# Kernel optimization log

Hardware: AMD Instinct MI355X
Metric: run time of the kernel (lower is better)

Reference implementation:

```python
import jax, jax.numpy as jnp
import numpy as np

N = 8192  # input_size
DT = 1.0
TAU1, TAU2, TAU3 = 20.0, 50.0, 100.0


def _corr(a, b):
    # Pearson correlation of two equal-length vectors (torch.corrcoef[0,1]), NaN -> 0
    ac = a - jnp.mean(a)
    bc = b - jnp.mean(b)
    c = jnp.sum(ac * bc) / jnp.sqrt(jnp.sum(ac * ac) * jnp.sum(bc * bc))
    return jnp.where(jnp.isnan(c), jnp.zeros_like(c), c)


def setup_inputs() -> dict:
    key = jax.random.key(0)
    ks = jax.random.split(key, 8)
    return {
        'sensory_motor_input': jax.random.normal(ks[0], (N,), jnp.float32),
        'layer1_state': jax.random.normal(ks[1], (N,), jnp.float32),
        'layer2_state': jax.random.normal(ks[2], (N // 2,), jnp.float32),
        'layer3_state': jax.random.normal(ks[3], (N // 4,), jnp.float32),
        'w12': jax.random.normal(ks[4], (N // 2, N), jnp.float32) * 0.1,
        'w23': jax.random.normal(ks[5], (N // 4, N // 2), jnp.float32) * 0.1,
        'w32': jax.random.normal(ks[6], (N // 2, N // 4), jnp.float32) * 0.1,
        'w21': jax.random.normal(ks[7], (N, N // 2), jnp.float32) * 0.1,
        'correlation_strength': jnp.zeros((), jnp.float32),
        'neural_coherence': jnp.zeros((), jnp.float32),
    }


def reference(sensory_motor_input, layer1_state, layer2_state, layer3_state,
              w12, w23, w32, w21, correlation_strength, neural_coherence):
    # Layer 1: direct sensorimotor, exponential decay toward tanh target
    l1_target = jnp.tanh(sensory_motor_input)
    d1 = 1.0 - DT / TAU1
    l1 = d1 * layer1_state + (1.0 - d1) * l1_target

    # Layer 2: bottom-up + 0.3 * top-down feedback
    l2_in = w12 @ l1 + 0.3 * (w32 @ layer3_state)
    d2 = 1.0 - DT / TAU2
    l2 = d2 * layer2_state + (1.0 - d2) * jnp.tanh(l2_in)

    # Layer 3: meta feedback
    d3 = 1.0 - DT / TAU3
    l3 = d3 * layer3_state + (1.0 - d3) * jnp.tanh(w23 @ l2)

    # Cross-layer correlations (truncate the larger vector)
    c12 = _corr(l1[: l2.shape[0]], l2)
    c23 = _corr(l2[: l3.shape[0]], l3)
    corr_new = 0.9 * correlation_strength + 0.1 * (c12 + c23) / 2.0

    total_activity = jnp.sum(jnp.abs(l1)) + jnp.sum(jnp.abs(l2)) + jnp.sum(jnp.abs(l3))
    activity_variance = jnp.var(jnp.concatenate([l1, l2, l3]), ddof=1)  # torch.var unbiased
    coherence = total_activity / (activity_variance + 1e-6)
    coh_new = 0.9 * neural_coherence + 0.1 * jnp.clip(coherence, 0.0, 10.0)

    hier_activity = total_activity / (N + N // 2 + N // 4)
    return (l1, l2, l3, corr_new, coh_new, hier_activity)
```

## Files before the change

### kernel.cpp

```cpp
#include <hip/hip_runtime.h>
#include <math.h>

#define N1 8192
#define N2 4096
#define N3 2048

typedef float f4 __attribute__((ext_vector_type(4)));

__global__ __launch_bounds__(256) void k_pre(const float* __restrict__ smi,
                                             const float* __restrict__ l1s,
                                             float* __restrict__ l1,
                                             const float* __restrict__ w32,
                                             const float* __restrict__ l3s,
                                             float* __restrict__ t2) {
    const int b = blockIdx.x;
    const int t = threadIdx.x;
    if (b < 32) {
        const int i = b * 256 + t;
        l1[i] = 0.95f * l1s[i] + 0.05f * tanhf(smi[i]);
        return;
    }
    __shared__ float ws[4][4];
    const int r0 = (b - 32) * 4;
    const f4* __restrict__ w0 = reinterpret_cast<const f4*>(w32) + (size_t)r0 * (N3 / 4);
    const f4* __restrict__ w1 = w0 + (N3 / 4);
    const f4* __restrict__ w2 = w1 + (N3 / 4);
    const f4* __restrict__ w3 = w2 + (N3 / 4);
    const f4* __restrict__ x = reinterpret_cast<const f4*>(l3s);

    float a0 = 0.f, a1 = 0.f, a2 = 0.f, a3 = 0.f;
#pragma unroll
    for (int k = 0; k < (N3 / 4) / 256; ++k) {
        const int i = t + k * 256;
        f4 xv = x[i];
        f4 u0 = __builtin_nontemporal_load(&w0[i]);
        f4 u1 = __builtin_nontemporal_load(&w1[i]);
        f4 u2 = __builtin_nontemporal_load(&w2[i]);
        f4 u3 = __builtin_nontemporal_load(&w3[i]);
        a0 = fmaf(u0.x, xv.x, fmaf(u0.y, xv.y, fmaf(u0.z, xv.z, fmaf(u0.w, xv.w, a0))));
        a1 = fmaf(u1.x, xv.x, fmaf(u1.y, xv.y, fmaf(u1.z, xv.z, fmaf(u1.w, xv.w, a1))));
        a2 = fmaf(u2.x, xv.x, fmaf(u2.y, xv.y, fmaf(u2.z, xv.z, fmaf(u2.w, xv.w, a2))));
        a3 = fmaf(u3.x, xv.x, fmaf(u3.y, xv.y, fmaf(u3.z, xv.z, fmaf(u3.w, xv.w, a3))));
    }
#pragma unroll
    for (int off = 32; off; off >>= 1) {
        a0 += __shfl_down(a0, off, 64);
        a1 += __shfl_down(a1, off, 64);
        a2 += __shfl_down(a2, off, 64);
        a3 += __shfl_down(a3, off, 64);
    }
    if ((t & 63) == 0) {
        const int w = t >> 6;
        ws[w][0] = a0; ws[w][1] = a1; ws[w][2] = a2; ws[w][3] = a3;
    }
    __syncthreads();
    if (t < 4) {
        t2[r0 + t] = ws[0][t] + ws[1][t] + ws[2][t] + ws[3][t];
    }
}

__global__ __launch_bounds__(256) void k_l2(const float* __restrict__ w12,
                                            const float* __restrict__ l1,
                                            const float* __restrict__ t2,
                                            const float* __restrict__ l2s,
                                            float* __restrict__ l2) {
    __shared__ float ws[4][4];
    const int r0 = blockIdx.x * 4;
    const int t = threadIdx.x;
    const f4* __restrict__ w0 = reinterpret_cast<const f4*>(w12) + (size_t)r0 * (N1 / 4);
    const f4* __restrict__ w1 = w0 + (N1 / 4);
    const f4* __restrict__ w2 = w1 + (N1 / 4);
    const f4* __restrict__ w3 = w2 + (N1 / 4);
    const f4* __restrict__ x = reinterpret_cast<const f4*>(l1);

    float a0 = 0.f, a1 = 0.f, a2 = 0.f, a3 = 0.f;
#pragma unroll
    for (int k = 0; k < (N1 / 4) / 256; ++k) {
        const int i = t + k * 256;
        f4 xv = x[i];
        f4 u0 = __builtin_nontemporal_load(&w0[i]);
        f4 u1 = __builtin_nontemporal_load(&w1[i]);
        f4 u2 = __builtin_nontemporal_load(&w2[i]);
        f4 u3 = __builtin_nontemporal_load(&w3[i]);
        a0 = fmaf(u0.x, xv.x, fmaf(u0.y, xv.y, fmaf(u0.z, xv.z, fmaf(u0.w, xv.w, a0))));
        a1 = fmaf(u1.x, xv.x, fmaf(u1.y, xv.y, fmaf(u1.z, xv.z, fmaf(u1.w, xv.w, a1))));
        a2 = fmaf(u2.x, xv.x, fmaf(u2.y, xv.y, fmaf(u2.z, xv.z, fmaf(u2.w, xv.w, a2))));
        a3 = fmaf(u3.x, xv.x, fmaf(u3.y, xv.y, fmaf(u3.z, xv.z, fmaf(u3.w, xv.w, a3))));
    }
#pragma unroll
    for (int off = 32; off; off >>= 1) {
        a0 += __shfl_down(a0, off, 64);
        a1 += __shfl_down(a1, off, 64);
        a2 += __shfl_down(a2, off, 64);
        a3 += __shfl_down(a3, off, 64);
    }
    if ((t & 63) == 0) {
        const int w = t >> 6;
        ws[w][0] = a0; ws[w][1] = a1; ws[w][2] = a2; ws[w][3] = a3;
    }
    __syncthreads();
    if (t < 4) {
        const int r = r0 + t;
        float tot = ws[0][t] + ws[1][t] + ws[2][t] + ws[3][t] + 0.3f * t2[r];
        l2[r] = 0.98f * l2s[r] + 0.02f * tanhf(tot);
    }
}

__global__ __launch_bounds__(256) void k_l3(const float* __restrict__ w23,
                                            const float* __restrict__ l2,
                                            const float* __restrict__ l3s,
                                            float* __restrict__ l3) {
    __shared__ float ws[4][4];
    const int r0 = blockIdx.x * 4;
    const int t = threadIdx.x;
    const f4* __restrict__ w0 = reinterpret_cast<const f4*>(w23) + (size_t)r0 * (N2 / 4);
    const f4* __restrict__ w1 = w0 + (N2 / 4);
    const f4* __restrict__ w2 = w1 + (N2 / 4);
    const f4* __restrict__ w3 = w2 + (N2 / 4);
    const f4* __restrict__ x = reinterpret_cast<const f4*>(l2);

    float a0 = 0.f, a1 = 0.f, a2 = 0.f, a3 = 0.f;
#pragma unroll
    for (int k = 0; k < (N2 / 4) / 256; ++k) {
        const int i = t + k * 256;
        f4 xv = x[i];
        f4 u0 = __builtin_nontemporal_load(&w0[i]);
        f4 u1 = __builtin_nontemporal_load(&w1[i]);
        f4 u2 = __builtin_nontemporal_load(&w2[i]);
        f4 u3 = __builtin_nontemporal_load(&w3[i]);
        a0 = fmaf(u0.x, xv.x, fmaf(u0.y, xv.y, fmaf(u0.z, xv.z, fmaf(u0.w, xv.w, a0))));
        a1 = fmaf(u1.x, xv.x, fmaf(u1.y, xv.y, fmaf(u1.z, xv.z, fmaf(u1.w, xv.w, a1))));
        a2 = fmaf(u2.x, xv.x, fmaf(u2.y, xv.y, fmaf(u2.z, xv.z, fmaf(u2.w, xv.w, a2))));
        a3 = fmaf(u3.x, xv.x, fmaf(u3.y, xv.y, fmaf(u3.z, xv.z, fmaf(u3.w, xv.w, a3))));
    }
#pragma unroll
    for (int off = 32; off; off >>= 1) {
        a0 += __shfl_down(a0, off, 64);
        a1 += __shfl_down(a1, off, 64);
        a2 += __shfl_down(a2, off, 64);
        a3 += __shfl_down(a3, off, 64);
    }
    if ((t & 63) == 0) {
        const int w = t >> 6;
        ws[w][0] = a0; ws[w][1] = a1; ws[w][2] = a2; ws[w][3] = a3;
    }
    __syncthreads();
    if (t < 4) {
        const int r = r0 + t;
        float tot = ws[0][t] + ws[1][t] + ws[2][t] + ws[3][t];
        l3[r] = 0.99f * l3s[r] + 0.01f * tanhf(tot);
    }
}

__global__ __launch_bounds__(1024) void k_fin(const float* __restrict__ out,
                                              const float* __restrict__ corr_in,
                                              const float* __restrict__ coh_in,
                                              float* __restrict__ scal) {
    __shared__ double sred[16][13];
    __shared__ double fin[13];
    const int t = threadIdx.x;
    const f4* __restrict__ o4 = reinterpret_cast<const f4*>(out);

    double p[13];
#pragma unroll
    for (int j = 0; j < 13; ++j) p[j] = 0.0;

    for (int i = t; i < 3584; i += 1024) {
        f4 v = o4[i];
#pragma unroll
        for (int c = 0; c < 4; ++c) {
            double d = (double)v[c];
            p[0] += fabs(d); p[1] += d; p[2] += d * d;
        }
    }
    {
        f4 x = o4[t];
        f4 y = o4[2048 + t];
#pragma unroll
        for (int c = 0; c < 4; ++c) {
            double dx = (double)x[c], dy = (double)y[c];
            p[3] += dx; p[4] += dy; p[5] += dx * dx; p[6] += dy * dy; p[7] += dx * dy;
        }
    }
    if (t < 512) {
        f4 x = o4[2048 + t];
        f4 y = o4[3072 + t];
#pragma unroll
        for (int c = 0; c < 4; ++c) {
            double dx = (double)x[c], dy = (double)y[c];
            p[8] += dx; p[9] += dy; p[10] += dx * dx; p[11] += dy * dy; p[12] += dx * dy;
        }
    }

#pragma unroll
    for (int j = 0; j < 13; ++j) {
        double v = p[j];
#pragma unroll
        for (int off = 32; off; off >>= 1) v += __shfl_down(v, off, 64);
        p[j] = v;
    }
    if ((t & 63) == 0) {
        const int w = t >> 6;
#pragma unroll
        for (int j = 0; j < 13; ++j) sred[w][j] = p[j];
    }
    __syncthreads();
    if (t < 13) {
        double s = 0.0;
#pragma unroll
        for (int w = 0; w < 16; ++w) s += sred[w][t];
        fin[t] = s;
    }
    __syncthreads();

    if (t == 0) {
        const double n12 = (double)N2;
        const double n23 = (double)N3;
        const double nall = (double)(N1 + N2 + N3);

        double sxy12 = fin[7] - fin[3] * fin[4] / n12;
        double sxx12 = fin[5] - fin[3] * fin[3] / n12;
        double syy12 = fin[6] - fin[4] * fin[4] / n12;
        double den12 = sqrt(sxx12 * syy12);
        double c12 = (den12 > 0.0 && isfinite(den12)) ? sxy12 / den12 : 0.0;

        double sxy23 = fin[12] - fin[8] * fin[9] / n23;
        double sxx23 = fin[10] - fin[8] * fin[8] / n23;
        double syy23 = fin[11] - fin[9] * fin[9] / n23;
        double den23 = sqrt(sxx23 * syy23);
        double c23 = (den23 > 0.0 && isfinite(den23)) ? sxy23 / den23 : 0.0;

        double corr_new = 0.9 * (double)corr_in[0] + 0.1 * (c12 + c23) * 0.5;

        double total = fin[0];
        double var = (fin[2] - fin[1] * fin[1] / nall) / (nall - 1.0);
        double coh = total / (var + 1e-6);
        coh = fmin(fmax(coh, 0.0), 10.0);
        double coh_new = 0.9 * (double)coh_in[0] + 0.1 * coh;

        scal[0] = (float)corr_new;
        scal[1] = (float)coh_new;
        scal[2] = (float)(total / nall);
    }
}

extern "C" void kernel_launch(void* const* d_in, const int* in_sizes, int n_in,
                              void* d_out, int out_size, void* d_ws, size_t ws_size,
                              hipStream_t stream) {
    const float* smi     = (const float*)d_in[0];
    const float* l1s     = (const float*)d_in[1];
    const float* l2s     = (const float*)d_in[2];
    const float* l3s     = (const float*)d_in[3];
    const float* w12     = (const float*)d_in[4];
    const float* w23     = (const float*)d_in[5];
    const float* w32     = (const float*)d_in[6];
    const float* corr_in = (const float*)d_in[8];
    const float* coh_in  = (const float*)d_in[9];

    float* out = (float*)d_out;
    float* l1 = out;
    float* l2 = out + N1;
    float* l3 = out + N1 + N2;
    float* scal = out + N1 + N2 + N3;
    float* t2 = (float*)d_ws;

    k_pre<<<dim3(32 + N2 / 4), dim3(256), 0, stream>>>(smi, l1s, l1, w32, l3s, t2);
    k_l2<<<dim3(N2 / 4), dim3(256), 0, stream>>>(w12, l1, t2, l2s, l2);
    k_l3<<<dim3(N3 / 4), dim3(256), 0, stream>>>(w23, l2, l3s, l3);
    k_fin<<<dim3(1), dim3(1024), 0, stream>>>(out, corr_in, coh_in, scal);
}
```

Baseline: 48.43 us.

## Fuse layer-1 update and top-down GEMV into layer-2 kernel; halve rows per l3 block

Merges the pre kernel (layer-1 tanh update plus the w32·l3 GEMV) into the layer-2 GEMV kernel. Every block now recomputes the full layer-1 vector into LDS, and the feedback term is folded into the per-thread partial sums before the reduction. This removes one launch and the global round trip for l1 and the t2 workspace. The cost is redundant tanh work and a 32KB LDS allocation per block, which limits occupancy. The layer-3 kernel now handles 2 rows per block instead of 4, doubling its grid for more parallelism.

```diff
diff --git a/kernel.cpp b/kernel.cpp
--- a/kernel.cpp
+++ b/kernel.cpp
@@ -7,32 +7,73 @@
 
 typedef float f4 __attribute__((ext_vector_type(4)));
 
-__global__ __launch_bounds__(256) void k_pre(const float* __restrict__ smi,
+__global__ __launch_bounds__(256) void k_l12(const float* __restrict__ smi,
                                              const float* __restrict__ l1s,
-                                             float* __restrict__ l1,
+                                             const float* __restrict__ w12,
                                              const float* __restrict__ w32,
                                              const float* __restrict__ l3s,
-                                             float* __restrict__ t2) {
-    const int b = blockIdx.x;
+                                             const float* __restrict__ l2s,
+                                             float* __restrict__ l1_out,
+                                             float* __restrict__ l2_out) {
+    __shared__ float lds_l1[N1];
+    __shared__ float ws[4][4];
     const int t = threadIdx.x;
-    if (b < 32) {
-        const int i = b * 256 + t;
-        l1[i] = 0.95f * l1s[i] + 0.05f * tanhf(smi[i]);
-        return;
-    }
-    __shared__ float ws[4][4];
-    const int r0 = (b - 32) * 4;
-    const f4* __restrict__ w0 = reinterpret_cast<const f4*>(w32) + (size_t)r0 * (N3 / 4);
-    const f4* __restrict__ w1 = w0 + (N3 / 4);
-    const f4* __restrict__ w2 = w1 + (N3 / 4);
-    const f4* __restrict__ w3 = w2 + (N3 / 4);
-    const f4* __restrict__ x = reinterpret_cast<const f4*>(l3s);
-
-    float a0 = 0.f, a1 = 0.f, a2 = 0.f, a3 = 0.f;
+    const int r0 = blockIdx.x * 4;
+
+    const f4* __restrict__ v0 = reinterpret_cast<const f4*>(w32) + (size_t)r0 * (N3 / 4);
+    const f4* __restrict__ v1 = v0 + (N3 / 4);
+    const f4* __restrict__ v2 = v1 + (N3 / 4);
+    const f4* __restrict__ v3 = v2 + (N3 / 4);
+    const f4* __restrict__ x3 = reinterpret_cast<const f4*>(l3s);
+    float b0 = 0.f, b1 = 0.f, b2 = 0.f, b3 = 0.f;
 #pragma unroll
     for (int k = 0; k < (N3 / 4) / 256; ++k) {
         const int i = t + k * 256;
-        f4 xv = x[i];
+        f4 xv = x3[i];
+        f4 u0 = __builtin_nontemporal_load(&v0[i]);
+        f4 u1 = __builtin_nontemporal_load(&v1[i]);
+        f4 u2 = __builtin_nontemporal_load(&v2[i]);
+        f4 u3 = __builtin_nontemporal_load(&v3[i]);
+        b0 = fmaf(u0.x, xv.x, fmaf(u0.y, xv.y, fmaf(u0.z, xv.z, fmaf(u0.w, xv.w, b0))));
+        b1 = fmaf(u1.x, xv.x, fmaf(u1.y, xv.y, fmaf(u1.z, xv.z, fmaf(u1.w, xv.w, b1))));
+        b2 = fmaf(u2.x, xv.x, fmaf(u2.y, xv.y, fmaf(u2.z, xv.z, fmaf(u2.w, xv.w, b2))));
+        b3 = fmaf(u3.x, xv.x, fmaf(u3.y, xv.y, fmaf(u3.z, xv.z, fmaf(u3.w, xv.w, b3))));
+    }
+
+    {
+        const f4* __restrict__ s4 = reinterpret_cast<const f4*>(smi);
+        const f4* __restrict__ p4 = reinterpret_cast<const f4*>(l1s);
+        f4* __restrict__ d4 = reinterpret_cast<f4*>(lds_l1);
+#pragma unroll
+        for (int k = 0; k < (N1 / 4) / 256; ++k) {
+            const int i = t + k * 256;
+            f4 s = s4[i];
+            f4 p = p4[i];
+            f4 r;
+            r.x = fmaf(0.95f, p.x, 0.05f * tanhf(s.x));
+            r.y = fmaf(0.95f, p.y, 0.05f * tanhf(s.y));
+            r.z = fmaf(0.95f, p.z, 0.05f * tanhf(s.z));
+            r.w = fmaf(0.95f, p.w, 0.05f * tanhf(s.w));
+            d4[i] = r;
+        }
+    }
+    __syncthreads();
+
+    if (blockIdx.x < 32) {
+        const int i = blockIdx.x * 256 + t;
+        l1_out[i] = lds_l1[i];
+    }
+
+    const f4* __restrict__ w0 = reinterpret_cast<const f4*>(w12) + (size_t)r0 * (N1 / 4);
+    const f4* __restrict__ w1 = w0 + (N1 / 4);
+    const f4* __restrict__ w2 = w1 + (N1 / 4);
+    const f4* __restrict__ w3 = w2 + (N1 / 4);
+    const f4* __restrict__ x1 = reinterpret_cast<const f4*>(lds_l1);
+    float a0 = 0.f, a1 = 0.f, a2 = 0.f, a3 = 0.f;
+#pragma unroll
+    for (int k = 0; k < (N1 / 4) / 256; ++k) {
+        const int i = t + k * 256;
+        f4 xv = x1[i];
         f4 u0 = __builtin_nontemporal_load(&w0[i]);
         f4 u1 = __builtin_nontemporal_load(&w1[i]);
         f4 u2 = __builtin_nontemporal_load(&w2[i]);
@@ -42,67 +83,27 @@
         a2 = fmaf(u2.x, xv.x, fmaf(u2.y, xv.y, fmaf(u2.z, xv.z, fmaf(u2.w, xv.w, a2))));
         a3 = fmaf(u3.x, xv.x, fmaf(u3.y, xv.y, fmaf(u3.z, xv.z, fmaf(u3.w, xv.w, a3))));
     }
+
+    float c0 = fmaf(0.3f, b0, a0);
+    float c1 = fmaf(0.3f, b1, a1);
+    float c2 = fmaf(0.3f, b2, a2);
+    float c3 = fmaf(0.3f, b3, a3);
 #pragma unroll
     for (int off = 32; off; off >>= 1) {
-        a0 += __shfl_down(a0, off, 64);
-        a1 += __shfl_down(a1, off, 64);
-        a2 += __shfl_down(a2, off, 64);
-        a3 += __shfl_down(a3, off, 64);
+        c0 += __shfl_down(c0, off, 64);
+        c1 += __shfl_down(c1, off, 64);
+        c2 += __shfl_down(c2, off, 64);
+        c3 += __shfl_down(c3, off, 64);
     }
     if ((t & 63) == 0) {
         const int w = t >> 6;
-        ws[w][0] = a0; ws[w][1] = a1; ws[w][2] = a2; ws[w][3] = a3;
-    }
-    __syncthreads();
-    if (t < 4) {
-        t2[r0 + t] = ws[0][t] + ws[1][t] + ws[2][t] + ws[3][t];
-    }
-}
-
-__global__ __launch_bounds__(256) void k_l2(const float* __restrict__ w12,
-                                            const float* __restrict__ l1,
-                                            const float* __restrict__ t2,
-                                            const float* __restrict__ l2s,
-                                            float* __restrict__ l2) {
-    __shared__ float ws[4][4];
-    const int r0 = blockIdx.x * 4;
-    const int t = threadIdx.x;
-    const f4* __restrict__ w0 = reinterpret_cast<const f4*>(w12) + (size_t)r0 * (N1 / 4);
-    const f4* __restrict__ w1 = w0 + (N1 / 4);
-    const f4* __restrict__ w2 = w1 + (N1 / 4);
-    const f4* __restrict__ w3 = w2 + (N1 / 4);
-    const f4* __restrict__ x = reinterpret_cast<const f4*>(l1);
-
-    float a0 = 0.f, a1 = 0.f, a2 = 0.f, a3 = 0.f;
-#pragma unroll
-    for (int k = 0; k < (N1 / 4) / 256; ++k) {
-        const int i = t + k * 256;
-        f4 xv = x[i];
-        f4 u0 = __builtin_nontemporal_load(&w0[i]);
-        f4 u1 = __builtin_nontemporal_load(&w1[i]);
-        f4 u2 = __builtin_nontemporal_load(&w2[i]);
-        f4 u3 = __builtin_nontemporal_load(&w3[i]);
-        a0 = fmaf(u0.x, xv.x, fmaf(u0.y, xv.y, fmaf(u0.z, xv.z, fmaf(u0.w, xv.w, a0))));
-        a1 = fmaf(u1.x, xv.x, fmaf(u1.y, xv.y, fmaf(u1.z, xv.z, fmaf(u1.w, xv.w, a1))));
-        a2 = fmaf(u2.x, xv.x, fmaf(u2.y, xv.y, fmaf(u2.z, xv.z, fmaf(u2.w, xv.w, a2))));
-        a3 = fmaf(u3.x, xv.x, fmaf(u3.y, xv.y, fmaf(u3.z, xv.z, fmaf(u3.w, xv.w, a3))));
-    }
-#pragma unroll
-    for (int off = 32; off; off >>= 1) {
-        a0 += __shfl_down(a0, off, 64);
-        a1 += __shfl_down(a1, off, 64);
-        a2 += __shfl_down(a2, off, 64);
-        a3 += __shfl_down(a3, off, 64);
-    }
-    if ((t & 63) == 0) {
-        const int w = t >> 6;
-        ws[w][0] = a0; ws[w][1] = a1; ws[w][2] = a2; ws[w][3] = a3;
+        ws[w][0] = c0; ws[w][1] = c1; ws[w][2] = c2; ws[w][3] = c3;
     }
     __syncthreads();
     if (t < 4) {
         const int r = r0 + t;
-        float tot = ws[0][t] + ws[1][t] + ws[2][t] + ws[3][t] + 0.3f * t2[r];
-        l2[r] = 0.98f * l2s[r] + 0.02f * tanhf(tot);
+        float tot = ws[0][t] + ws[1][t] + ws[2][t] + ws[3][t];
+        l2_out[r] = 0.98f * l2s[r] + 0.02f * tanhf(tot);
     }
 }
 
@@ -110,42 +111,31 @@
                                             const float* __restrict__ l2,
                                             const float* __restrict__ l3s,
                                             float* __restrict__ l3) {
-    __shared__ float ws[4][4];
-    const int r0 = blockIdx.x * 4;
+    __shared__ float ws[4][2];
+    const int r0 = blockIdx.x * 2;
     const int t = threadIdx.x;
     const f4* __restrict__ w0 = reinterpret_cast<const f4*>(w23) + (size_t)r0 * (N2 / 4);
     const f4* __restrict__ w1 = w0 + (N2 / 4);
-    const f4* __restrict__ w2 = w1 + (N2 / 4);
-    const f4* __restrict__ w3 = w2 + (N2 / 4);
-    const f4* __restrict__ x = reinterpret_cast<const f4*>(l2);
-
-    float a0 = 0.f, a1 = 0.f, a2 = 0.f, a3 = 0.f;
+    const f4* __restrict__ x2 = reinterpret_cast<const f4*>(l2);
+
+    float a0 = 0.f, a1 = 0.f;
 #pragma unroll
     for (int k = 0; k < (N2 / 4) / 256; ++k) {
         const int i = t + k * 256;
-        f4 xv = x[i];
+        f4 xv = x2[i];
         f4 u0 = __builtin_nontemporal_load(&w0[i]);
         f4 u1 = __builtin_nontemporal_load(&w1[i]);
-        f4 u2 = __builtin_nontemporal_load(&w2[i]);
-        f4 u3 = __builtin_nontemporal_load(&w3[i]);
         a0 = fmaf(u0.x, xv.x, fmaf(u0.y, xv.y, fmaf(u0.z, xv.z, fmaf(u0.w, xv.w, a0))));
         a1 = fmaf(u1.x, xv.x, fmaf(u1.y, xv.y, fmaf(u1.z, xv.z, fmaf(u1.w, xv.w, a1))));
-        a2 = fmaf(u2.x, xv.x, fmaf(u2.y, xv.y, fmaf(u2.z, xv.z, fmaf(u2.w, xv.w, a2))));
-        a3 = fmaf(u3.x, xv.x, fmaf(u3.y, xv.y, fmaf(u3.z, xv.z, fmaf(u3.w, xv.w, a3))));
     }
 #pragma unroll
     for (int off = 32; off; off >>= 1) {
         a0 += __shfl_down(a0, off, 64);
         a1 += __shfl_down(a1, off, 64);
-        a2 += __shfl_down(a2, off, 64);
-        a3 += __shfl_down(a3, off, 64);
-    }
-    if ((t & 63) == 0) {
-        const int w = t >> 6;
-        ws[w][0] = a0; ws[w][1] = a1; ws[w][2] = a2; ws[w][3] = a3;
-    }
-    __syncthreads();
-    if (t < 4) {
+    }
+    if ((t & 63) == 0) { ws[t >> 6][0] = a0; ws[t >> 6][1] = a1; }
+    __syncthreads();
+    if (t < 2) {
         const int r = r0 + t;
         float tot = ws[0][t] + ws[1][t] + ws[2][t] + ws[3][t];
         l3[r] = 0.99f * l3s[r] + 0.01f * tanhf(tot);
@@ -262,10 +252,8 @@
     float* l2 = out + N1;
     float* l3 = out + N1 + N2;
     float* scal = out + N1 + N2 + N3;
-    float* t2 = (float*)d_ws;
-
-    k_pre<<<dim3(32 + N2 / 4), dim3(256), 0, stream>>>(smi, l1s, l1, w32, l3s, t2);
-    k_l2<<<dim3(N2 / 4), dim3(256), 0, stream>>>(w12, l1, t2, l2s, l2);
-    k_l3<<<dim3(N3 / 4), dim3(256), 0, stream>>>(w23, l2, l3s, l3);
+
+    k_l12<<<dim3(N2 / 4), dim3(256), 0, stream>>>(smi, l1s, w12, w32, l3s, l2s, l1, l2);
+    k_l3<<<dim3(N3 / 2), dim3(256), 0, stream>>>(w23, l2, l3s, l3);
     k_fin<<<dim3(1), dim3(1024), 0, stream>>>(out, corr_in, coh_in, scal);
 }
```

Result: no change. 49.05 us (+1.3%).
